# Optimization experiments

Measured on AMD Instinct MI355X. Metric: run time of the kernel, lower is better.

Reference implementation:

```python
import jax, jax.numpy as jnp
import numpy as np

HID, H, VD = 512, 8, 64
SCALE = 1.0 / np.sqrt(VD).astype(np.float32)


def setup_inputs() -> dict:
    key = jax.random.key(0)
    ks = jax.random.split(key, 9)
    B, S = 2, 2048
    std = 1.0 / np.sqrt(HID).astype(np.float32)
    return {
        "sequences": jax.random.normal(ks[0], (B, S, HID), jnp.float32),
        "Wq": jax.random.normal(ks[1], (H, HID, VD), jnp.float32) * std,
        "bq": jax.random.normal(ks[2], (H, VD), jnp.float32) * std,
        "Wk": jax.random.normal(ks[3], (H, HID, VD), jnp.float32) * std,
        "bk": jax.random.normal(ks[4], (H, VD), jnp.float32) * std,
        "Wv": jax.random.normal(ks[5], (H, HID, VD), jnp.float32) * std,
        "bv": jax.random.normal(ks[6], (H, VD), jnp.float32) * std,
        "Wo": jax.random.normal(ks[7], (HID, HID), jnp.float32) * std,
        "bo": jax.random.normal(ks[8], (HID,), jnp.float32) * std,
    }


def reference(sequences, Wq, bq, Wk, bk, Wv, bv, Wo, bo):
    # Batched equivalent of the per-sequence / per-head Python loops:
    # q,k,v: [B, H, S, VD]
    q = jnp.einsum("bsd,hde->bhse", sequences, Wq) + bq[None, :, None, :]
    k = jnp.einsum("bsd,hde->bhse", sequences, Wk) + bk[None, :, None, :]
    v = jnp.einsum("bsd,hde->bhse", sequences, Wv) + bv[None, :, None, :]
    scores = jax.nn.softmax(jnp.einsum("bhse,bhte->bhst", q, k) * SCALE, axis=-1)
    z = jnp.einsum("bhst,bhte->bhse", scores, v)  # [B,H,S,VD]
    # concat heads along feature dim -> [B, S, HID]
    B, _, S, _ = z.shape
    z = jnp.transpose(z, (0, 2, 1, 3)).reshape(B, S, HID)
    return z @ Wo + bo
```

## Files before the change

### kernel.cpp

```cpp
#include <hip/hip_runtime.h>
#include <hip/hip_fp16.h>

#define HID 512
#define NH 8
#define VD 64
#define SEQ 2048
#define NB 2
#define MTOT (NB*SEQ)
#define LOG2E 1.4426950408889634f
#define QSCALE (0.125f * LOG2E)

typedef _Float16 f16x8 __attribute__((ext_vector_type(8)));
typedef _Float16 f16x4 __attribute__((ext_vector_type(4)));
typedef float f32x4 __attribute__((ext_vector_type(4)));

#define OFF_SEQH  (0u)
#define SZ_SEQH   ((unsigned)(MTOT*HID*2))
#define OFF_WT    (OFF_SEQH + SZ_SEQH)
#define SZ_WT     ((unsigned)(3*NH*VD*HID*2))
#define OFF_WOT   (OFF_WT + SZ_WT)
#define SZ_WOT    ((unsigned)(HID*HID*2))
#define OFF_BIAS  (OFF_WOT + SZ_WOT)
#define SZ_BIAS   ((unsigned)(3*NH*VD*4))
#define OFF_Q     (OFF_BIAS + SZ_BIAS)
#define SZ_QKV    ((unsigned)(NB*NH*SEQ*VD*2))
#define OFF_K     (OFF_Q + SZ_QKV)
#define OFF_VT    (OFF_K + SZ_QKV)
#define OFF_Z     (OFF_VT + SZ_QKV)

__device__ __forceinline__ int swz(int row, int g) {
    return row*128 + ((g ^ (row & 7)) << 4);
}
__device__ __forceinline__ int swz256(int row, int g) {
    return row*256 + ((g ^ (row & 7)) << 4);
}

__device__ __forceinline__ void gload16(const void* g, void* l) {
    __builtin_amdgcn_global_load_lds(
        (const __attribute__((address_space(1))) unsigned int*)g,
        (__attribute__((address_space(3))) unsigned int*)l, 16, 0, 0);
}

__global__ __launch_bounds__(256) void k_convert(
    const float* __restrict__ seq,
    const float* __restrict__ Wq, const float* __restrict__ Wk,
    const float* __restrict__ Wv, const float* __restrict__ Wo,
    char* __restrict__ ws)
{
    __shared__ _Float16 lt[64][72];
    int bx = blockIdx.x, tid = threadIdx.x;

    if (bx < 192) {
        int z = bx / 64, h = (bx & 63) >> 3, kt = bx & 7;
        const float* W = (z==0) ? Wq : (z==1 ? Wk : Wv);
        int k0 = kt*64;
        #pragma unroll
        for (int p = 0; p < 4; ++p) {
            int flat = p*256 + tid;
            int kr = flat >> 4, c4 = flat & 15;
            float4 v = *(const float4*)(W + (h*HID + k0 + kr)*VD + c4*4);
            lt[c4*4+0][kr] = (_Float16)v.x;
            lt[c4*4+1][kr] = (_Float16)v.y;
            lt[c4*4+2][kr] = (_Float16)v.z;
            lt[c4*4+3][kr] = (_Float16)v.w;
        }
        __syncthreads();
        _Float16* wt = (_Float16*)(ws + OFF_WT);
        #pragma unroll
        for (int p = 0; p < 2; ++p) {
            int flat = p*256 + tid;
            int vd = flat >> 3, gg = flat & 7;
            f16x8 o;
            #pragma unroll
            for (int j = 0; j < 8; ++j) o[j] = lt[vd][gg*8+j];
            *(f16x8*)(wt + ((z*NH + h)*VD + vd)*HID + k0 + gg*8) = o;
        }
    } else if (bx < 256) {
        int idx = bx - 192, ntile = idx >> 3, kt = idx & 7;
        int k0 = kt*64, n0 = ntile*64;
        #pragma unroll
        for (int p = 0; p < 4; ++p) {
            int flat = p*256 + tid;
            int kr = flat >> 4, c4 = flat & 15;
            float4 v = *(const float4*)(Wo + (k0 + kr)*HID + n0 + c4*4);
            lt[c4*4+0][kr] = (_Float16)v.x;
            lt[c4*4+1][kr] = (_Float16)v.y;
            lt[c4*4+2][kr] = (_Float16)v.z;
            lt[c4*4+3][kr] = (_Float16)v.w;
        }
        __syncthreads();
        _Float16* wot = (_Float16*)(ws + OFF_WOT);
        #pragma unroll
        for (int p = 0; p < 2; ++p) {
            int flat = p*256 + tid;
            int nl = flat >> 3, gg = flat & 7;
            f16x8 o;
            #pragma unroll
            for (int j = 0; j < 8; ++j) o[j] = lt[nl][gg*8+j];
            *(f16x8*)(wot + (n0 + nl)*HID + k0 + gg*8) = o;
        }
    } else {
        int t = (bx - 256)*256 + tid;
        const float4* s4p = (const float4*)seq;
        f16x4* d = (f16x4*)(ws + OFF_SEQH);
        for (int i = t; i < MTOT*HID/4; i += 256*256) {
            float4 v = s4p[i];
            f16x4 o = {(_Float16)v.x,(_Float16)v.y,(_Float16)v.z,(_Float16)v.w};
            d[i] = o;
        }
    }
}

__global__ __launch_bounds__(256) void k_proj(char* __restrict__ ws,
    const float* __restrict__ bq, const float* __restrict__ bk,
    const float* __restrict__ bv)
{
    __shared__ uint4 smem4[1536];
    char* smem = (char*)smem4;
    const _Float16* seqh = (const _Float16*)(ws + OFF_SEQH);
    const _Float16* wt   = (const _Float16*)(ws + OFF_WT);

    int m0 = blockIdx.x * 128;
    int h  = blockIdx.y;
    int z  = blockIdx.z;
    int tid = threadIdx.x, lane = tid & 63, w = tid >> 6;
    const float* bias = (z==0) ? bq : (z==1 ? bk : bv);

    f32x4 acc[2][4] = {};

    for (int kt = 0; kt < HID/64; ++kt) {
        #pragma unroll
        for (int p = 0; p < 4; ++p) {
            int flat = p*256 + tid; int row = flat >> 3, g = flat & 7;
            uint4 v = *(const uint4*)(seqh + (m0+row)*HID + kt*64 + g*8);
            *(uint4*)(smem + swz(row, g)) = v;
        }
        #pragma unroll
        for (int p = 0; p < 2; ++p) {
            int flat = p*256 + tid; int n = flat >> 3, g = flat & 7;
            uint4 v = *(const uint4*)(wt + ((z*NH+h)*VD + n)*HID + kt*64 + g*8);
            *(uint4*)(smem + 16384 + swz(n, g)) = v;
        }
        __syncthreads();
        #pragma unroll
        for (int kf = 0; kf < 2; ++kf) {
            f16x8 a[2], b[4];
            #pragma unroll
            for (int mf = 0; mf < 2; ++mf) {
                int row = w*32 + mf*16 + (lane & 15);
                a[mf] = *(const f16x8*)(smem + swz(row, kf*4 + (lane>>4)));
            }
            #pragma unroll
            for (int nf = 0; nf < 4; ++nf) {
                int n = nf*16 + (lane & 15);
                b[nf] = *(const f16x8*)(smem + 16384 + swz(n, kf*4 + (lane>>4)));
            }
            #pragma unroll
            for (int mf = 0; mf < 2; ++mf)
                #pragma unroll
                for (int nf = 0; nf < 4; ++nf)
                    acc[mf][nf] = __builtin_amdgcn_mfma_f32_16x16x32_f16(
                        a[mf], b[nf], acc[mf][nf], 0, 0, 0);
        }
        __syncthreads();
    }

    int bb = m0 >> 11;
    int s0 = m0 & (SEQ-1);

    if (z < 2) {
        float sc = (z == 0) ? QSCALE : 1.0f;
        _Float16* out = (_Float16*)(ws + (z==0 ? OFF_Q : OFF_K));
        #pragma unroll
        for (int mf = 0; mf < 2; ++mf)
            #pragma unroll
            for (int nf = 0; nf < 4; ++nf)
                #pragma unroll
                for (int r = 0; r < 4; ++r) {
                    int mrow = w*32 + mf*16 + ((lane>>4)<<2) + r;
                    int col  = nf*16 + (lane & 15);
                    float v = (acc[mf][nf][r] + bias[h*VD + col]) * sc;
                    out[((bb*NH+h)*SEQ + s0 + mrow)*VD + col] = (_Float16)v;
                }
    } else {
        _Float16* sT = (_Float16*)smem;
        #pragma unroll
        for (int mf = 0; mf < 2; ++mf)
            #pragma unroll
            for (int nf = 0; nf < 4; ++nf)
                #pragma unroll
                for (int r = 0; r < 4; ++r) {
                    int srow = w*32 + mf*16 + ((lane>>4)<<2) + r;
                    int vd   = nf*16 + (lane & 15);
                    float v = acc[mf][nf][r] + bias[h*VD + vd];
                    sT[vd*128 + srow] = (_Float16)v;
                }
        __syncthreads();
        _Float16* vt = (_Float16*)(ws + OFF_VT);
        #pragma unroll
        for (int p = 0; p < 4; ++p) {
            int flat = p*256 + tid; int vd = flat >> 4, g = flat & 15;
            uint4 v = *(const uint4*)((char*)sT + vd*256 + g*16);
            *(uint4*)(vt + ((bb*NH+h)*VD + vd)*SEQ + s0 + g*8) = v;
        }
    }
}

__global__ __launch_bounds__(256, 2) void k_attn(char* __restrict__ ws)
{
    __shared__ uint4 smem4[5120];
    char* smem = (char*)smem4;
    const int OP = 65536;

    int m0 = blockIdx.x * 64;
    int bh = blockIdx.y;
    int tid = threadIdx.x, lane = tid & 63, w = tid >> 6;

    const char* KbB  = (const char*)(ws + OFF_K)  + (size_t)bh*SEQ*VD*2;
    const char* VtbB = (const char*)(ws + OFF_VT) + (size_t)bh*VD*SEQ*2;
    const _Float16* Qb = (const _Float16*)(ws + OFF_Q) + (size_t)bh*SEQ*VD;
    _Float16* Zp = (_Float16*)(ws + OFF_Z);

    int krow_base = w*8  + (lane >> 3);
    int kg        = lane & 7;
    int vvd_base  = w*4  + (lane >> 4);
    int vg        = lane & 15;

    #define STAGE(t0_, buf_)                                                   \
    {                                                                          \
        const int OKb = (buf_)*16384, OVb = 32768 + (buf_)*16384;              \
        _Pragma("unroll")                                                      \
        for (int p = 0; p < 4; ++p) {                                          \
            int krow = p*32 + krow_base;                                       \
            gload16(KbB + (size_t)((t0_) + krow)*128 + ((kg ^ (krow & 7))<<4), \
                    smem + OKb + (p*4 + w)*1024);                              \
            int vvd = p*16 + vvd_base;                                         \
            gload16(VtbB + (size_t)vvd*(SEQ*2) + (t0_)*2                       \
                         + ((vg ^ (vvd & 7))<<4),                              \
                    smem + OVb + (p*4 + w)*1024);                              \
        }                                                                      \
    }

    f16x8 aq[2];
    #pragma unroll
    for (int kf = 0; kf < 2; ++kf)
        aq[kf] = *(const f16x8*)(Qb + (m0 + w*16 + (lane & 15))*VD
                                 + kf*32 + (lane>>4)*8);

    float lrun[4] = {0.f, 0.f, 0.f, 0.f};
    f32x4 zacc[4] = {};

    STAGE(0, 0);

    int cur = 0;
    for (int t0 = 0; t0 < SEQ; t0 += 128) {
        __syncthreads();

        if (t0 + 128 < SEQ) STAGE(t0 + 128, cur^1);

        const int OK = cur*16384, OV = 32768 + cur*16384;

        f32x4 sacc[8] = {};
        #pragma unroll
        for (int kf = 0; kf < 2; ++kf) {
            f16x8 bk_[8];
            #pragma unroll
            for (int nf = 0; nf < 8; ++nf) {
                int trow = nf*16 + (lane & 15);
                bk_[nf] = *(const f16x8*)(smem + OK + swz(trow, kf*4 + (lane>>4)));
            }
            #pragma unroll
            for (int nf = 0; nf < 8; ++nf)
                sacc[nf] = __builtin_amdgcn_mfma_f32_16x16x32_f16(
                    aq[kf], bk_[nf], sacc[nf], 0, 0, 0);
        }

        #pragma unroll
        for (int r = 0; r < 4; ++r) {
            float s = 0.f;
            #pragma unroll
            for (int nf = 0; nf < 8; ++nf) {
                float p = __builtin_amdgcn_exp2f(sacc[nf][r]);
                sacc[nf][r] = p;
                s += p;
            }
            #pragma unroll
            for (int d = 1; d < 16; d <<= 1) s += __shfl_xor(s, d, 64);
            lrun[r] += s;
        }

        #pragma unroll
        for (int nf = 0; nf < 8; ++nf)
            #pragma unroll
            for (int r = 0; r < 4; ++r) {
                int row = w*16 + ((lane>>4)<<2) + r;
                int g   = nf*2 + ((lane>>3) & 1);
                *(_Float16*)(smem + OP + row*256 + ((g ^ (row & 7))<<4)
                             + (lane & 7)*2) = (_Float16)sacc[nf][r];
            }

        #pragma unroll
        for (int kf = 0; kf < 4; ++kf) {
            int prow = w*16 + (lane & 15);
            f16x8 ap = *(const f16x8*)(smem + OP + swz256(prow, kf*4 + (lane>>4)));
            f16x8 bv_[4];
            #pragma unroll
            for (int nf = 0; nf < 4; ++nf) {
                int vd = nf*16 + (lane & 15);
                bv_[nf] = *(const f16x8*)(smem + OV + swz256(vd, kf*4 + (lane>>4)));
            }
            #pragma unroll
            for (int nf = 0; nf < 4; ++nf)
                zacc[nf] = __builtin_amdgcn_mfma_f32_16x16x32_f16(
                    ap, bv_[nf], zacc[nf], 0, 0, 0);
        }

        cur ^= 1;
    }
    #undef STAGE

    int bb = bh >> 3, h = bh & 7;
    float linv[4];
    #pragma unroll
    for (int r = 0; r < 4; ++r) linv[r] = 1.0f / lrun[r];
    #pragma unroll
    for (int nf = 0; nf < 4; ++nf)
        #pragma unroll
        for (int r = 0; r < 4; ++r) {
            int s  = m0 + w*16 + ((lane>>4)<<2) + r;
            int vd = nf*16 + (lane & 15);
            float v = zacc[nf][r] * linv[r];
            Zp[((size_t)(bb*SEQ + s))*HID + h*VD + vd] = (_Float16)v;
        }
}

__global__ __launch_bounds__(256) void k_outproj(const char* __restrict__ ws,
                                                 const float* __restrict__ bo,
                                                 float* __restrict__ out)
{
    __shared__ uint4 smem4[1536];
    char* smem = (char*)smem4;
    const _Float16* Zp  = (const _Float16*)(ws + OFF_Z);
    const _Float16* wot = (const _Float16*)(ws + OFF_WOT);

    int m0 = blockIdx.x * 128;
    int n0 = blockIdx.y * 64;
    int tid = threadIdx.x, lane = tid & 63, w = tid >> 6;

    f32x4 acc[2][4] = {};

    for (int kt = 0; kt < HID/64; ++kt) {
        #pragma unroll
        for (int p = 0; p < 4; ++p) {
            int flat = p*256 + tid; int row = flat >> 3, g = flat & 7;
            uint4 v = *(const uint4*)(Zp + (m0+row)*HID + kt*64 + g*8);
            *(uint4*)(smem + swz(row, g)) = v;
        }
        #pragma unroll
        for (int p = 0; p < 2; ++p) {
            int flat = p*256 + tid; int n = flat >> 3, g = flat & 7;
            uint4 v = *(const uint4*)(wot + (n0+n)*HID + kt*64 + g*8);
            *(uint4*)(smem + 16384 + swz(n, g)) = v;
        }
        __syncthreads();
        #pragma unroll
        for (int kf = 0; kf < 2; ++kf) {
            f16x8 a[2], b[4];
            #pragma unroll
            for (int mf = 0; mf < 2; ++mf) {
                int row = w*32 + mf*16 + (lane & 15);
                a[mf] = *(const f16x8*)(smem + swz(row, kf*4 + (lane>>4)));
            }
            #pragma unroll
            for (int nf = 0; nf < 4; ++nf) {
                int n = nf*16 + (lane & 15);
                b[nf] = *(const f16x8*)(smem + 16384 + swz(n, kf*4 + (lane>>4)));
            }
            #pragma unroll
            for (int mf = 0; mf < 2; ++mf)
                #pragma unroll
                for (int nf = 0; nf < 4; ++nf)
                    acc[mf][nf] = __builtin_amdgcn_mfma_f32_16x16x32_f16(
                        a[mf], b[nf], acc[mf][nf], 0, 0, 0);
        }
        __syncthreads();
    }

    #pragma unroll
    for (int mf = 0; mf < 2; ++mf)
        #pragma unroll
        for (int nf = 0; nf < 4; ++nf)
            #pragma unroll
            for (int r = 0; r < 4; ++r) {
                int mrow = m0 + w*32 + mf*16 + ((lane>>4)<<2) + r;
                int col  = n0 + nf*16 + (lane & 15);
                out[(unsigned)mrow*HID + col] = acc[mf][nf][r] + bo[col];
            }
}

extern "C" void kernel_launch(void* const* d_in, const int* in_sizes, int n_in,
                              void* d_out, int out_size, void* d_ws, size_t ws_size,
                              hipStream_t stream)
{
    const float* seq = (const float*)d_in[0];
    const float* Wq  = (const float*)d_in[1];
    const float* bq  = (const float*)d_in[2];
    const float* Wk  = (const float*)d_in[3];
    const float* bk  = (const float*)d_in[4];
    const float* Wv  = (const float*)d_in[5];
    const float* bv  = (const float*)d_in[6];
    const float* Wo  = (const float*)d_in[7];
    const float* bo  = (const float*)d_in[8];
    char* ws = (char*)d_ws;
    float* out = (float*)d_out;

    k_convert<<<dim3(512), dim3(256), 0, stream>>>(seq, Wq, Wk, Wv, Wo, ws);
    k_proj<<<dim3(32, 8, 3), dim3(256), 0, stream>>>(ws, bq, bk, bv);
    k_attn<<<dim3(32, 16), dim3(256), 0, stream>>>(ws);
    k_outproj<<<dim3(32, 8), dim3(256), 0, stream>>>(ws, bo, out);
}
```

Baseline: 138.2 us.

## Fuse seq fp16 conversion into QKV projection and widen projection tiles

The separate fp32-to-fp16 conversion of the input sequence is removed, and k_proj now loads fp32 rows and converts them while staging into shared memory. k_proj computes Q, K and V for one head in a single block with a 192-wide N tile, so each seq tile is read once instead of three times. k_outproj's N tile grows from 64 to 128. This cuts global traffic and launch work, but the larger accumulator arrays (24 and 16 MFMA tiles) raise register pressure and the grids become small (256 and 128 blocks), which may lower occupancy.

```diff
diff --git a/kernel.cpp b/kernel.cpp
--- a/kernel.cpp
+++ b/kernel.cpp
@@ -14,15 +14,11 @@
 typedef _Float16 f16x4 __attribute__((ext_vector_type(4)));
 typedef float f32x4 __attribute__((ext_vector_type(4)));
 
-#define OFF_SEQH  (0u)
-#define SZ_SEQH   ((unsigned)(MTOT*HID*2))
-#define OFF_WT    (OFF_SEQH + SZ_SEQH)
+#define OFF_WT    (0u)
 #define SZ_WT     ((unsigned)(3*NH*VD*HID*2))
 #define OFF_WOT   (OFF_WT + SZ_WT)
 #define SZ_WOT    ((unsigned)(HID*HID*2))
-#define OFF_BIAS  (OFF_WOT + SZ_WOT)
-#define SZ_BIAS   ((unsigned)(3*NH*VD*4))
-#define OFF_Q     (OFF_BIAS + SZ_BIAS)
+#define OFF_Q     (OFF_WOT + SZ_WOT)
 #define SZ_QKV    ((unsigned)(NB*NH*SEQ*VD*2))
 #define OFF_K     (OFF_Q + SZ_QKV)
 #define OFF_VT    (OFF_K + SZ_QKV)
@@ -42,7 +38,6 @@
 }
 
 __global__ __launch_bounds__(256) void k_convert(
-    const float* __restrict__ seq,
     const float* __restrict__ Wq, const float* __restrict__ Wk,
     const float* __restrict__ Wv, const float* __restrict__ Wo,
     char* __restrict__ ws)
@@ -75,7 +70,7 @@
             for (int j = 0; j < 8; ++j) o[j] = lt[vd][gg*8+j];
             *(f16x8*)(wt + ((z*NH + h)*VD + vd)*HID + k0 + gg*8) = o;
         }
-    } else if (bx < 256) {
+    } else {
         int idx = bx - 192, ntile = idx >> 3, kt = idx & 7;
         int k0 = kt*64, n0 = ntile*64;
         #pragma unroll
@@ -99,66 +94,61 @@
             for (int j = 0; j < 8; ++j) o[j] = lt[nl][gg*8+j];
             *(f16x8*)(wot + (n0 + nl)*HID + k0 + gg*8) = o;
         }
-    } else {
-        int t = (bx - 256)*256 + tid;
-        const float4* s4p = (const float4*)seq;
-        f16x4* d = (f16x4*)(ws + OFF_SEQH);
-        for (int i = t; i < MTOT*HID/4; i += 256*256) {
-            float4 v = s4p[i];
-            f16x4 o = {(_Float16)v.x,(_Float16)v.y,(_Float16)v.z,(_Float16)v.w};
-            d[i] = o;
-        }
-    }
-}
-
-__global__ __launch_bounds__(256) void k_proj(char* __restrict__ ws,
+    }
+}
+
+__global__ __launch_bounds__(256) void k_proj(const float* __restrict__ seq,
+    char* __restrict__ ws,
     const float* __restrict__ bq, const float* __restrict__ bk,
     const float* __restrict__ bv)
 {
-    __shared__ uint4 smem4[1536];
+    __shared__ uint4 smem4[2560];
     char* smem = (char*)smem4;
-    const _Float16* seqh = (const _Float16*)(ws + OFF_SEQH);
-    const _Float16* wt   = (const _Float16*)(ws + OFF_WT);
+    const _Float16* wt = (const _Float16*)(ws + OFF_WT);
 
     int m0 = blockIdx.x * 128;
     int h  = blockIdx.y;
-    int z  = blockIdx.z;
     int tid = threadIdx.x, lane = tid & 63, w = tid >> 6;
-    const float* bias = (z==0) ? bq : (z==1 ? bk : bv);
-
-    f32x4 acc[2][4] = {};
+
+    f32x4 acc[2][12] = {};
 
     for (int kt = 0; kt < HID/64; ++kt) {
         #pragma unroll
         for (int p = 0; p < 4; ++p) {
             int flat = p*256 + tid; int row = flat >> 3, g = flat & 7;
-            uint4 v = *(const uint4*)(seqh + (m0+row)*HID + kt*64 + g*8);
-            *(uint4*)(smem + swz(row, g)) = v;
-        }
-        #pragma unroll
-        for (int p = 0; p < 2; ++p) {
+            const float* src = seq + (size_t)(m0+row)*HID + kt*64 + g*8;
+            float4 v0 = *(const float4*)(src);
+            float4 v1 = *(const float4*)(src + 4);
+            f16x8 o = {(_Float16)v0.x,(_Float16)v0.y,(_Float16)v0.z,(_Float16)v0.w,
+                       (_Float16)v1.x,(_Float16)v1.y,(_Float16)v1.z,(_Float16)v1.w};
+            *(f16x8*)(smem + swz(row, g)) = o;
+        }
+        #pragma unroll
+        for (int p = 0; p < 6; ++p) {
             int flat = p*256 + tid; int n = flat >> 3, g = flat & 7;
-            uint4 v = *(const uint4*)(wt + ((z*NH+h)*VD + n)*HID + kt*64 + g*8);
+            int z = n >> 6, vd = n & 63;
+            uint4 v = *(const uint4*)(wt + ((size_t)(z*NH+h)*VD + vd)*HID
+                                      + kt*64 + g*8);
             *(uint4*)(smem + 16384 + swz(n, g)) = v;
         }
         __syncthreads();
         #pragma unroll
         for (int kf = 0; kf < 2; ++kf) {
-            f16x8 a[2], b[4];
+            f16x8 a[2], b[12];
             #pragma unroll
             for (int mf = 0; mf < 2; ++mf) {
                 int row = w*32 + mf*16 + (lane & 15);
                 a[mf] = *(const f16x8*)(smem + swz(row, kf*4 + (lane>>4)));
             }
             #pragma unroll
-            for (int nf = 0; nf < 4; ++nf) {
+            for (int nf = 0; nf < 12; ++nf) {
                 int n = nf*16 + (lane & 15);
                 b[nf] = *(const f16x8*)(smem + 16384 + swz(n, kf*4 + (lane>>4)));
             }
             #pragma unroll
             for (int mf = 0; mf < 2; ++mf)
                 #pragma unroll
-                for (int nf = 0; nf < 4; ++nf)
+                for (int nf = 0; nf < 12; ++nf)
                     acc[mf][nf] = __builtin_amdgcn_mfma_f32_16x16x32_f16(
                         a[mf], b[nf], acc[mf][nf], 0, 0, 0);
         }
@@ -168,9 +158,11 @@
     int bb = m0 >> 11;
     int s0 = m0 & (SEQ-1);
 
-    if (z < 2) {
-        float sc = (z == 0) ? QSCALE : 1.0f;
-        _Float16* out = (_Float16*)(ws + (z==0 ? OFF_Q : OFF_K));
+    #pragma unroll
+    for (int z = 0; z < 2; ++z) {
+        const float* bias = z ? bk : bq;
+        float sc = z ? 1.0f : QSCALE;
+        _Float16* outp = (_Float16*)(ws + (z==0 ? OFF_Q : OFF_K));
         #pragma unroll
         for (int mf = 0; mf < 2; ++mf)
             #pragma unroll
@@ -179,30 +171,30 @@
                 for (int r = 0; r < 4; ++r) {
                     int mrow = w*32 + mf*16 + ((lane>>4)<<2) + r;
                     int col  = nf*16 + (lane & 15);
-                    float v = (acc[mf][nf][r] + bias[h*VD + col]) * sc;
-                    out[((bb*NH+h)*SEQ + s0 + mrow)*VD + col] = (_Float16)v;
+                    float v = (acc[mf][z*4+nf][r] + bias[h*VD + col]) * sc;
+                    outp[((bb*NH+h)*SEQ + s0 + mrow)*VD + col] = (_Float16)v;
                 }
-    } else {
-        _Float16* sT = (_Float16*)smem;
-        #pragma unroll
-        for (int mf = 0; mf < 2; ++mf)
-            #pragma unroll
-            for (int nf = 0; nf < 4; ++nf)
-                #pragma unroll
-                for (int r = 0; r < 4; ++r) {
-                    int srow = w*32 + mf*16 + ((lane>>4)<<2) + r;
-                    int vd   = nf*16 + (lane & 15);
-                    float v = acc[mf][nf][r] + bias[h*VD + vd];
-                    sT[vd*128 + srow] = (_Float16)v;
-                }
-        __syncthreads();
-        _Float16* vt = (_Float16*)(ws + OFF_VT);
-        #pragma unroll
-        for (int p = 0; p < 4; ++p) {
-            int flat = p*256 + tid; int vd = flat >> 4, g = flat & 15;
-            uint4 v = *(const uint4*)((char*)sT + vd*256 + g*16);
-            *(uint4*)(vt + ((bb*NH+h)*VD + vd)*SEQ + s0 + g*8) = v;
-        }
+    }
+
+    _Float16* sT = (_Float16*)smem;
+    #pragma unroll
+    for (int mf = 0; mf < 2; ++mf)
+        #pragma unroll
+        for (int nf = 0; nf < 4; ++nf)
+            #pragma unroll
+            for (int r = 0; r < 4; ++r) {
+                int srow = w*32 + mf*16 + ((lane>>4)<<2) + r;
+                int vd   = nf*16 + (lane & 15);
+                float v = acc[mf][8+nf][r] + bv[h*VD + vd];
+                sT[vd*128 + srow] = (_Float16)v;
+            }
+    __syncthreads();
+    _Float16* vt = (_Float16*)(ws + OFF_VT);
+    #pragma unroll
+    for (int p = 0; p < 4; ++p) {
+        int flat = p*256 + tid; int vd = flat >> 4, g = flat & 15;
+        uint4 v = *(const uint4*)((char*)sT + vd*256 + g*16);
+        *(uint4*)(vt + ((size_t)(bb*NH+h)*VD + vd)*SEQ + s0 + g*8) = v;
     }
 }
 
@@ -338,48 +330,48 @@
                                                  const float* __restrict__ bo,
                                                  float* __restrict__ out)
 {
-    __shared__ uint4 smem4[1536];
+    __shared__ uint4 smem4[2048];
     char* smem = (char*)smem4;
     const _Float16* Zp  = (const _Float16*)(ws + OFF_Z);
     const _Float16* wot = (const _Float16*)(ws + OFF_WOT);
 
     int m0 = blockIdx.x * 128;
-    int n0 = blockIdx.y * 64;
+    int n0 = blockIdx.y * 128;
     int tid = threadIdx.x, lane = tid & 63, w = tid >> 6;
 
-    f32x4 acc[2][4] = {};
+    f32x4 acc[2][8] = {};
 
     for (int kt = 0; kt < HID/64; ++kt) {
         #pragma unroll
         for (int p = 0; p < 4; ++p) {
             int flat = p*256 + tid; int row = flat >> 3, g = flat & 7;
-            uint4 v = *(const uint4*)(Zp + (m0+row)*HID + kt*64 + g*8);
+            uint4 v = *(const uint4*)(Zp + (size_t)(m0+row)*HID + kt*64 + g*8);
             *(uint4*)(smem + swz(row, g)) = v;
         }
         #pragma unroll
-        for (int p = 0; p < 2; ++p) {
+        for (int p = 0; p < 4; ++p) {
             int flat = p*256 + tid; int n = flat >> 3, g = flat & 7;
-            uint4 v = *(const uint4*)(wot + (n0+n)*HID + kt*64 + g*8);
+            uint4 v = *(const uint4*)(wot + (size_t)(n0+n)*HID + kt*64 + g*8);
             *(uint4*)(smem + 16384 + swz(n, g)) = v;
         }
         __syncthreads();
         #pragma unroll
         for (int kf = 0; kf < 2; ++kf) {
-            f16x8 a[2], b[4];
+            f16x8 a[2], b[8];
             #pragma unroll
             for (int mf = 0; mf < 2; ++mf) {
                 int row = w*32 + mf*16 + (lane & 15);
                 a[mf] = *(const f16x8*)(smem + swz(row, kf*4 + (lane>>4)));
             }
             #pragma unroll
-            for (int nf = 0; nf < 4; ++nf) {
+            for (int nf = 0; nf < 8; ++nf) {
                 int n = nf*16 + (lane & 15);
                 b[nf] = *(const f16x8*)(smem + 16384 + swz(n, kf*4 + (lane>>4)));
             }
             #pragma unroll
             for (int mf = 0; mf < 2; ++mf)
                 #pragma unroll
-                for (int nf = 0; nf < 4; ++nf)
+                for (int nf = 0; nf < 8; ++nf)
                     acc[mf][nf] = __builtin_amdgcn_mfma_f32_16x16x32_f16(
                         a[mf], b[nf], acc[mf][nf], 0, 0, 0);
         }
@@ -389,12 +381,12 @@
     #pragma unroll
     for (int mf = 0; mf < 2; ++mf)
         #pragma unroll
-        for (int nf = 0; nf < 4; ++nf)
+        for (int nf = 0; nf < 8; ++nf)
             #pragma unroll
             for (int r = 0; r < 4; ++r) {
                 int mrow = m0 + w*32 + mf*16 + ((lane>>4)<<2) + r;
                 int col  = n0 + nf*16 + (lane & 15);
-                out[(unsigned)mrow*HID + col] = acc[mf][nf][r] + bo[col];
+                out[(size_t)mrow*HID + col] = acc[mf][nf][r] + bo[col];
             }
 }
 
@@ -414,8 +406,8 @@
     char* ws = (char*)d_ws;
     float* out = (float*)d_out;
 
-    k_convert<<<dim3(512), dim3(256), 0, stream>>>(seq, Wq, Wk, Wv, Wo, ws);
-    k_proj<<<dim3(32, 8, 3), dim3(256), 0, stream>>>(ws, bq, bk, bv);
+    k_convert<<<dim3(256), dim3(256), 0, stream>>>(Wq, Wk, Wv, Wo, ws);
+    k_proj<<<dim3(32, 8), dim3(256), 0, stream>>>(seq, ws, bq, bk, bv);
     k_attn<<<dim3(32, 16), dim3(256), 0, stream>>>(ws);
-    k_outproj<<<dim3(32, 8), dim3(256), 0, stream>>>(ws, bo, out);
-}
+    k_outproj<<<dim3(32, 4), dim3(256), 0, stream>>>(ws, bo, out);
+}
```

New measurement: 145.3 us. +5.1%, slower.
